# Kernel optimization log

Measured on AMD Instinct MI355X. Metric: run time of the kernel, lower is better.

The kernel has to match this reference:

```python
import jax, jax.numpy as jnp
import numpy as np

QUERY_DIM = 512
CTX_DIM = 1576
N_VIEWS = 36


def get_pano_affinity_np():
    pano_a = np.eye(36, dtype=np.float64)
    for v in range(0, 12):
        pano_a[v, v + 12] = 1
        if v == 0:
            pano_a[v, 11] = 1; pano_a[v, 11 + 12] = 1
        else:
            pano_a[v, v - 1] = 1; pano_a[v, v - 1 + 12] = 1
        if v == 11:
            pano_a[v, 0] = 1; pano_a[v, 0 + 12] = 1
        else:
            pano_a[v, v + 1] = 1; pano_a[v, v + 1 + 12] = 1
    for v in range(12, 24):
        pano_a[v, v + 12] = 1; pano_a[v, v - 12] = 1
        if v == 12:
            pano_a[v, 23] = 1; pano_a[v, 23 + 12] = 1; pano_a[v, 23 - 12] = 1
        else:
            pano_a[v, v - 1] = 1; pano_a[v, v - 1 + 12] = 1; pano_a[v, v - 1 - 12] = 1
        if v == 23:
            pano_a[v, 12] = 1; pano_a[v, 12 + 12] = 1; pano_a[v, 12 - 12] = 1
        else:
            pano_a[v, v + 1] = 1; pano_a[v, v + 1 + 12] = 1; pano_a[v, v + 1 - 12] = 1
    for v in range(24, 36):
        pano_a[v, v - 12] = 1
        if v == 24:
            pano_a[v, 35] = 1; pano_a[v, 35 - 12] = 1
        else:
            pano_a[v, v - 1] = 1; pano_a[v, v - 1 - 12] = 1
        if v == 35:
            pano_a[v, 24] = 1; pano_a[v, 24 - 12] = 1
        else:
            pano_a[v, v + 1] = 1; pano_a[v, v + 1 - 12] = 1
    # cv.GaussianBlur((3,3), sigma=0) uses fixed kernel [0.25,0.5,0.25];
    # BORDER_TRANSPARENT leaves border pixels unchanged.
    h = pano_a[:, :-2] * 0.25 + pano_a[:, 1:-1] * 0.5 + pano_a[:, 2:] * 0.25
    v2 = h[:-2] * 0.25 + h[1:-1] * 0.5 + h[2:] * 0.25
    out = pano_a.copy()
    out[1:-1, 1:-1] = v2
    out[np.eye(36, dtype=bool)] = 1.0
    out = out.astype(np.float32)
    out[out == 0] = 0.01
    return out


def setup_inputs() -> dict:
    key = jax.random.key(0)
    ks = jax.random.split(key, 8)
    B, L = 128, 8
    Q = jax.random.normal(ks[0], (B, L, QUERY_DIM), dtype=jnp.float32)
    V = jax.random.normal(ks[1], (B, L, N_VIEWS, CTX_DIM), dtype=jnp.float32)
    detect_feats = jax.random.normal(ks[2], (B, L, 900), dtype=jnp.float32)
    knowledge_vector = jax.random.normal(ks[3], (B, L, 112), dtype=jnp.float32)
    teacher_action_view_ids = jax.random.randint(ks[4], (B, L), 0, N_VIEWS, dtype=jnp.int64 if jax.config.jax_enable_x64 else jnp.int32)
    W_key = 0.02 * jax.random.normal(ks[5], (QUERY_DIM, 2476), dtype=jnp.float32)
    W_query = 0.02 * jax.random.normal(ks[6], (QUERY_DIM, QUERY_DIM), dtype=jnp.float32)
    W_out = 0.02 * jax.random.normal(ks[7], (QUERY_DIM, QUERY_DIM + CTX_DIM + 112), dtype=jnp.float32)
    return {"Q": Q, "V": V, "detect_feats": detect_feats,
            "knowledge_vector": knowledge_vector,
            "teacher_action_view_ids": teacher_action_view_ids,
            "W_key": W_key, "W_query": W_query, "W_out": W_out}


def reference(Q, V, detect_feats, knowledge_vector, teacher_action_view_ids,
              W_key, W_query, W_out):
    pano_a = jnp.asarray(get_pano_affinity_np())  # [36,36]
    B, L, qd = Q.shape
    ba = B * L
    Qf = Q.reshape(ba, qd) @ W_query.T                      # [ba, qd]
    Vf = V.reshape(ba, N_VIEWS, CTX_DIM)                    # [ba, 36, ctx]
    df = detect_feats.reshape(ba, 900)
    kv = knowledge_vector.reshape(ba, 112)
    tid = teacher_action_view_ids.reshape(ba)
    # K = Linear(cat(V, detect)) ; split the matmul to avoid materializing cat
    Wk_v, Wk_d = W_key[:, :CTX_DIM], W_key[:, CTX_DIM:]
    K = jnp.einsum('bnc,qc->bnq', Vf, Wk_v) + (df @ Wk_d.T)[:, None, :]  # [ba,36,qd]
    energy = jnp.einsum('bnq,bq->bn', K, Qf)                # [ba, 36]
    scale = qd ** (-0.5)
    attn = jax.nn.softmax(energy * scale, axis=1)           # [ba, 36]
    pano_tea = jax.lax.stop_gradient(pano_a[tid])           # [ba, 36]
    attn_gcn = attn * pano_tea
    weighted_context = jnp.einsum('bn,bnc->bc', attn_gcn, Vf)  # [ba, ctx]
    h = jnp.concatenate([weighted_context, Qf, kv], axis=1)
    h_tilde = jnp.tanh(h @ W_out.T)                         # [ba, qd]
    return (h_tilde, attn)
```

## Files before the change

kernel.cpp:

```cpp
#include <hip/hip_runtime.h>
#include <hip/hip_bf16.h>
#include <math.h>

typedef float f32x4 __attribute__((ext_vector_type(4)));
typedef short short8 __attribute__((ext_vector_type(8)));
typedef short short4v __attribute__((ext_vector_type(4)));

#define BA 1024
#define QD 512
#define CD 1576
#define NV 36
#define KVD 112
#define HLD 2200
#define WKLD 2476
#define CD4 394
#define LDP 72

__device__ __forceinline__ float pano_adj(int v, int w) {
    if (v == w) return 1.f;
    int rv = v / 12, rw = w / 12;
    int dr = rv - rw; if (dr < 0) dr = -dr;
    if (dr > 1) return 0.f;
    int dc = ((v % 12) - (w % 12) + 12) % 12;
    if (dc == 1 || dc == 11) return 1.f;
    if (dc == 0 && dr == 1) return 1.f;
    return 0.f;
}

__device__ __forceinline__ float pano_entry(int i, int j) {
    if (i == j) return 1.0f;
    float val;
    if (i >= 1 && i <= 34 && j >= 1 && j <= 34) {
        float wr[3] = {0.25f, 0.5f, 0.25f};
        val = 0.f;
        #pragma unroll
        for (int di = 0; di < 3; ++di)
            #pragma unroll
            for (int dj = 0; dj < 3; ++dj)
                val += wr[di] * wr[dj] * pano_adj(i - 1 + di, j - 1 + dj);
    } else {
        val = pano_adj(i, j);
    }
    return (val == 0.f) ? 0.01f : val;
}

__device__ __forceinline__ short f2bf(float f) {
    __hip_bfloat16 h = __float2bfloat16(f);
    union { __hip_bfloat16 b; short s; } u; u.b = h; return u.s;
}

template<bool ABF16, bool BBF16, bool CBF16, bool TANH>
__device__ void gemm_tile64(const void* __restrict__ Av, const void* __restrict__ Bv,
                            void* __restrict__ Cv, int m0, int n0, int N, int K,
                            int lda, int ldb, int ldc,
                            short* __restrict__ As, short* __restrict__ Bs) {
    const int t = threadIdx.x;
    const int lane = t & 63, w = t >> 6;
    const float* Af = (const float*)Av; const short* Ah = (const short*)Av;
    const float* Bf = (const float*)Bv; const short* Bh = (const short*)Bv;

    const int ar = t >> 3, akq = (t & 7) * 8;

    short8 abuf, bbuf;

    auto loadA = [&](int k0) {
        const size_t ro = (size_t)(m0 + ar) * lda;
        const int k = k0 + akq;
        short8 z;
        if (ABF16) {
            if (k + 8 <= K) z = *(const short8*)(Ah + ro + k);
            else {
                #pragma unroll
                for (int j = 0; j < 8; ++j) z[j] = (k + j < K) ? Ah[ro + k + j] : (short)0;
            }
        } else {
            if (k + 8 <= K) {
                f32x4 v0 = *(const f32x4*)(Af + ro + k);
                f32x4 v1 = *(const f32x4*)(Af + ro + k + 4);
                z[0]=f2bf(v0.x); z[1]=f2bf(v0.y); z[2]=f2bf(v0.z); z[3]=f2bf(v0.w);
                z[4]=f2bf(v1.x); z[5]=f2bf(v1.y); z[6]=f2bf(v1.z); z[7]=f2bf(v1.w);
            } else {
                #pragma unroll
                for (int j = 0; j < 8; ++j) z[j] = (k + j < K) ? f2bf(Af[ro + k + j]) : (short)0;
            }
        }
        abuf = z;
    };
    auto loadB = [&](int k0) {
        const int rn = n0 + ar;
        const size_t ro = (size_t)rn * ldb;
        const bool ok = rn < N;
        const int k = k0 + akq;
        short8 z;
        if (BBF16) {
            if (ok && k + 8 <= K) z = *(const short8*)(Bh + ro + k);
            else {
                #pragma unroll
                for (int j = 0; j < 8; ++j) z[j] = (ok && k + j < K) ? Bh[ro + k + j] : (short)0;
            }
        } else {
            if (ok && k + 8 <= K) {
                f32x4 v0 = *(const f32x4*)(Bf + ro + k);
                f32x4 v1 = *(const f32x4*)(Bf + ro + k + 4);
                z[0]=f2bf(v0.x); z[1]=f2bf(v0.y); z[2]=f2bf(v0.z); z[3]=f2bf(v0.w);
                z[4]=f2bf(v1.x); z[5]=f2bf(v1.y); z[6]=f2bf(v1.z); z[7]=f2bf(v1.w);
            } else {
                #pragma unroll
                for (int j = 0; j < 8; ++j) z[j] = (ok && k + j < K) ? f2bf(Bf[ro + k + j]) : (short)0;
            }
        }
        bbuf = z;
    };
    auto writeAB = [&](int buf) {
        *(short8*)&As[buf * (64 * LDP) + ar * LDP + akq] = abuf;
        *(short8*)&Bs[buf * (64 * LDP) + ar * LDP + akq] = bbuf;
    };

    const int wm = (w >> 2) * 32;
    const int wn = (w & 3) * 16;
    const int kb = (lane >> 4) * 8;
    int aidx[2], bidx;
    #pragma unroll
    for (int i = 0; i < 2; ++i)
        aidx[i] = (wm + i * 16 + (lane & 15)) * LDP + kb;
    bidx = (wn + (lane & 15)) * LDP + kb;

    f32x4 acc[2];
    #pragma unroll
    for (int i = 0; i < 2; ++i) acc[i] = (f32x4){0.f, 0.f, 0.f, 0.f};

    const int nk = (K + 63) / 64;
    loadA(0); loadB(0); writeAB(0);
    __syncthreads();

    int cur = 0;
    for (int kt = 0; kt < nk; ++kt) {
        const bool more = (kt + 1 < nk);
        if (more) { loadA((kt + 1) * 64); loadB((kt + 1) * 64); }

        #pragma unroll
        for (int ks = 0; ks < 2; ++ks) {
            short8 bfr = *(short8*)&Bs[cur * (64 * LDP) + bidx + ks * 32];
            #pragma unroll
            for (int i = 0; i < 2; ++i) {
                short8 afr = *(short8*)&As[cur * (64 * LDP) + aidx[i] + ks * 32];
                acc[i] = __builtin_amdgcn_mfma_f32_16x16x32_bf16(afr, bfr, acc[i], 0, 0, 0);
            }
        }
        if (more) writeAB(cur ^ 1);
        __syncthreads();
        cur ^= 1;
    }

    #pragma unroll
    for (int i = 0; i < 2; ++i) {
        int row = m0 + wm + i * 16 + (lane >> 4) * 4;
        int col = n0 + wn + (lane & 15);
        if (col < N) {
            #pragma unroll
            for (int r = 0; r < 4; ++r) {
                float v = acc[i][r];
                if (TANH) v = tanhf(v);
                if (CBF16) ((short*)Cv)[(size_t)(row + r) * ldc + col] = f2bf(v);
                else       ((float*)Cv)[(size_t)(row + r) * ldc + col] = v;
            }
        }
    }
}

__global__ __launch_bounds__(512) void gemm1_prep(
        const float* __restrict__ Q, const float* __restrict__ Wq,
        const float* __restrict__ Wk, const float* __restrict__ Wo,
        short* __restrict__ h, short* __restrict__ wk_t,
        short* __restrict__ wo_b) {
    __shared__ __align__(16) short As[2][64 * LDP];
    __shared__ __align__(16) short Bs[2][64 * LDP];
    __shared__ float tile[32][33];
    const int bx = blockIdx.x, t = threadIdx.x;

    if (bx < 128) {
        gemm_tile64<false, false, true, false>(
            (const void*)Q, (const void*)Wq, (void*)(h + CD),
            (bx >> 3) * 64, (bx & 7) * 64, QD, QD,
            QD, QD, HLD, &As[0][0], &Bs[0][0]);
    } else if (bx < 328) {
        const int pb = bx - 128;
        const int tx = t & 31, ty = t >> 5;
        for (int it = pb; it < 800; it += 200) {
            const int n0 = (it % 50) * 32, q0 = (it / 50) * 32;
            #pragma unroll
            for (int i = 0; i < 2; ++i)
                tile[ty + i * 16][tx] =
                    Wk[(size_t)(q0 + ty + i * 16) * WKLD + n0 + tx];
            __syncthreads();
            #pragma unroll
            for (int i = 0; i < 2; ++i) {
                int n = n0 + ty + i * 16;
                if (n < CD)
                    wk_t[(size_t)n * QD + q0 + tx] = f2bf(tile[tx][ty + i * 16]);
            }
            __syncthreads();
        }
    } else {
        const int NWO4 = (QD * HLD) / 4;
        for (int i = (bx - 328) * 512 + t; i < NWO4; i += 56 * 512) {
            f32x4 v4 = ((const f32x4*)Wo)[i];
            short4v o = { f2bf(v4.x), f2bf(v4.y), f2bf(v4.z), f2bf(v4.w) };
            ((short4v*)wo_b)[i] = o;
        }
    }
}

__global__ __launch_bounds__(256) void gemm2_nt(
        const short* __restrict__ Ah, const short* __restrict__ Bt,
        float* __restrict__ C, int M, int N, int K,
        int lda, int ldb, int ldc) {
    __shared__ __align__(16) short As[2][64 * LDP];
    __shared__ __align__(16) short Bs[2][64 * LDP];
    const int t = threadIdx.x;
    const int lane = t & 63, w = t >> 6;
    const int m0 = blockIdx.y * 64, n0 = blockIdx.x * 64;

    const int ar = t >> 2, akq = (t & 3) * 16;
    const int br = t >> 2, bkq = (t & 3) * 16;

    short8 abuf[2], bbuf[2];

    auto loadA = [&](int k0) {
        const size_t ro = (size_t)(m0 + ar) * lda;
        #pragma unroll
        for (int g = 0; g < 2; ++g) {
            int k = k0 + akq + g * 8;
            short8 z;
            if (k + 8 <= K) z = *(const short8*)(Ah + ro + k);
            else {
                #pragma unroll
                for (int j = 0; j < 8; ++j) z[j] = (k + j < K) ? Ah[ro + k + j] : (short)0;
            }
            abuf[g] = z;
        }
    };
    auto loadB = [&](int k0) {
        const int rn = n0 + br;
        const size_t ro = (size_t)rn * ldb;
        const bool ok = rn < N;
        #pragma unroll
        for (int g = 0; g < 2; ++g) {
            int k = k0 + bkq + g * 8;
            short8 z;
            if (ok && k + 8 <= K) z = *(const short8*)(Bt + ro + k);
            else {
                #pragma unroll
                for (int j = 0; j < 8; ++j) z[j] = (ok && k + j < K) ? Bt[ro + k + j] : (short)0;
            }
            bbuf[g] = z;
        }
    };
    auto writeAB = [&](int buf) {
        #pragma unroll
        for (int g = 0; g < 2; ++g) {
            *(short8*)&As[buf][ar * LDP + akq + g * 8] = abuf[g];
            *(short8*)&Bs[buf][br * LDP + bkq + g * 8] = bbuf[g];
        }
    };

    const int wm = (w >> 1) * 32, wn = (w & 1) * 32;
    const int kb = (lane >> 4) * 8;
    int aidx[2], bidx[2];
    #pragma unroll
    for (int i = 0; i < 2; ++i) {
        aidx[i] = (wm + i * 16 + (lane & 15)) * LDP + kb;
        bidx[i] = (wn + i * 16 + (lane & 15)) * LDP + kb;
    }

    f32x4 acc[2][2];
    #pragma unroll
    for (int i = 0; i < 2; ++i)
        #pragma unroll
        for (int j = 0; j < 2; ++j) acc[i][j] = (f32x4){0.f, 0.f, 0.f, 0.f};

    const int nk = (K + 63) / 64;
    loadA(0); loadB(0); writeAB(0);
    __syncthreads();

    int cur = 0;
    for (int kt = 0; kt < nk; ++kt) {
        const bool more = (kt + 1 < nk);
        if (more) { loadA((kt + 1) * 64); loadB((kt + 1) * 64); }

        #pragma unroll
        for (int ks = 0; ks < 2; ++ks) {
            short8 afr[2], bfr[2];
            #pragma unroll
            for (int i = 0; i < 2; ++i) afr[i] = *(short8*)&As[cur][aidx[i] + ks * 32];
            #pragma unroll
            for (int j = 0; j < 2; ++j) bfr[j] = *(short8*)&Bs[cur][bidx[j] + ks * 32];
            #pragma unroll
            for (int i = 0; i < 2; ++i)
                #pragma unroll
                for (int j = 0; j < 2; ++j)
                    acc[i][j] = __builtin_amdgcn_mfma_f32_16x16x32_bf16(afr[i], bfr[j], acc[i][j], 0, 0, 0);
        }
        if (more) writeAB(cur ^ 1);
        __syncthreads();
        cur ^= 1;
    }

    #pragma unroll
    for (int i = 0; i < 2; ++i) {
        #pragma unroll
        for (int j = 0; j < 2; ++j) {
            int row = m0 + wm + i * 16 + (lane >> 4) * 4;
            int col = n0 + wn + j * 16 + (lane & 15);
            if (col < N) {
                #pragma unroll
                for (int r = 0; r < 4; ++r)
                    C[(size_t)(row + r) * ldc + col] = acc[i][j][r];
            }
        }
    }
}

#define NR 5
#define NCH 7
__global__ __launch_bounds__(512, 2) void attn_wc_multib(
        const float* __restrict__ V, const float* __restrict__ P,
        const int* __restrict__ tid, const float* __restrict__ kv,
        short* __restrict__ h, float* __restrict__ attn_out) {
    const int t = threadIdx.x;
    const int w = t >> 6, lane = t & 63;
    __shared__ float en[NV];
    __shared__ float ag[NV];
    __shared__ __align__(16) f32x4 part[8 * 448];

    f32x4 p[NCH];
    f32x4 v[NR][NCH];

    auto issue_loads = [&](int b) {
        const f32x4* V4 = (const f32x4*)(V + (size_t)b * NV * CD);
        const f32x4* P4 = (const f32x4*)(P + (size_t)b * CD);
        #pragma unroll
        for (int j = 0; j < NCH; ++j) {
            int c = lane + 64 * j;
            p[j] = (c < CD4) ? P4[c] : (f32x4){0.f, 0.f, 0.f, 0.f};
        }
        #pragma unroll
        for (int r = 0; r < NR; ++r) {
            int n = w + 8 * r;
            #pragma unroll
            for (int j = 0; j < NCH; ++j) {
                int c = lane + 64 * j;
                v[r][j] = (n < NV && c < CD4) ? V4[(size_t)n * CD4 + c]
                                              : (f32x4){0.f, 0.f, 0.f, 0.f};
            }
        }
    };

    issue_loads(blockIdx.x * 4);

    for (int bi = 0; bi < 4; ++bi) {
        const int b = blockIdx.x * 4 + bi;

        #pragma unroll
        for (int r = 0; r < NR; ++r) {
            float s = 0.f;
            #pragma unroll
            for (int j = 0; j < NCH; ++j) {
                f32x4 vv = v[r][j], pp = p[j];
                s += vv.x * pp.x + vv.y * pp.y + vv.z * pp.z + vv.w * pp.w;
            }
            #pragma unroll
            for (int off = 32; off > 0; off >>= 1) s += __shfl_xor(s, off);
            int n = w + 8 * r;
            if (lane == 0 && n < NV) en[n] = s;
        }
        __syncthreads();

        if (t < 64) {
            const float SCALE = 0.044194173824159216f;
            float e = (t < NV) ? en[t] * SCALE : -1e30f;
            float m = e;
            #pragma unroll
            for (int off = 32; off > 0; off >>= 1) m = fmaxf(m, __shfl_xor(m, off));
            float pr = (t < NV) ? __expf(e - m) : 0.f;
            float s = pr;
            #pragma unroll
            for (int off = 32; off > 0; off >>= 1) s += __shfl_xor(s, off);
            float a = pr / s;
            if (t < NV) {
                attn_out[(size_t)b * NV + t] = a;
                ag[t] = a * pano_entry(tid[b], t);
            }
        }
        __syncthreads();

        f32x4 acc[NCH];
        #pragma unroll
        for (int j = 0; j < NCH; ++j) acc[j] = (f32x4){0.f, 0.f, 0.f, 0.f};
        #pragma unroll
        for (int r = 0; r < NR; ++r) {
            int n = w + 8 * r;
            float a = (n < NV) ? ag[n] : 0.f;
            #pragma unroll
            for (int j = 0; j < NCH; ++j) {
                acc[j].x += a * v[r][j].x; acc[j].y += a * v[r][j].y;
                acc[j].z += a * v[r][j].z; acc[j].w += a * v[r][j].w;
            }
        }
        #pragma unroll
        for (int j = 0; j < NCH; ++j)
            part[w * 448 + lane + 64 * j] = acc[j];

        if (bi < 3) issue_loads(b + 1);
        __syncthreads();

        short* hb = h + (size_t)b * HLD;
        if (t < CD4) {
            f32x4 s = part[t];
            #pragma unroll
            for (int w2 = 1; w2 < 8; ++w2) {
                f32x4 q = part[w2 * 448 + t];
                s.x += q.x; s.y += q.y; s.z += q.z; s.w += q.w;
            }
            short4v o = { f2bf(s.x), f2bf(s.y), f2bf(s.z), f2bf(s.w) };
            *(short4v*)(hb + t * 4) = o;
        }
        if (t < KVD)
            hb[CD + QD + t] = f2bf(kv[(size_t)b * KVD + t]);
    }
}

__global__ __launch_bounds__(256) void gemm4_tanh(
        const short* __restrict__ A, const short* __restrict__ B,
        float* __restrict__ C) {
    __shared__ __align__(16) short As[2][32 * LDP];
    __shared__ __align__(16) short Bs[2][32 * LDP];
    const int t = threadIdx.x;
    const int lane = t & 63, w = t >> 6;
    const int n0 = blockIdx.x * 32, m0 = blockIdx.y * 32;
    const int sr = t >> 3, skq = (t & 7) * 8;
    const int K = HLD;

    short8 abuf, bbuf;
    auto load = [&](int k0) {
        int k = k0 + skq;
        const short* pa = A + (size_t)(m0 + sr) * HLD + k;
        const short* pb = B + (size_t)(n0 + sr) * HLD + k;
        short8 za, zb;
        if (k + 8 <= K) { za = *(const short8*)pa; zb = *(const short8*)pb; }
        else {
            #pragma unroll
            for (int j = 0; j < 8; ++j) {
                za[j] = (k + j < K) ? pa[j] : (short)0;
                zb[j] = (k + j < K) ? pb[j] : (short)0;
            }
        }
        abuf = za; bbuf = zb;
    };
    auto write = [&](int buf) {
        *(short8*)&As[buf][sr * LDP + skq] = abuf;
        *(short8*)&Bs[buf][sr * LDP + skq] = bbuf;
    };

    const int wm = (w >> 1) * 16, wn = (w & 1) * 16;
    const int kb = (lane >> 4) * 8;
    const int aidx = (wm + (lane & 15)) * LDP + kb;
    const int bidx = (wn + (lane & 15)) * LDP + kb;

    f32x4 acc = {0.f, 0.f, 0.f, 0.f};
    const int nk = (K + 63) / 64;
    load(0); write(0);
    __syncthreads();

    int cur = 0;
    for (int kt = 0; kt < nk; ++kt) {
        const bool more = (kt + 1 < nk);
        if (more) load((kt + 1) * 64);

        #pragma unroll
        for (int ks = 0; ks < 2; ++ks) {
            short8 afr = *(short8*)&As[cur][aidx + ks * 32];
            short8 bfr = *(short8*)&Bs[cur][bidx + ks * 32];
            acc = __builtin_amdgcn_mfma_f32_16x16x32_bf16(afr, bfr, acc, 0, 0, 0);
        }
        if (more) write(cur ^ 1);
        __syncthreads();
        cur ^= 1;
    }

    const int row = m0 + wm + (lane >> 4) * 4;
    const int col = n0 + wn + (lane & 15);
    #pragma unroll
    for (int r = 0; r < 4; ++r)
        C[(size_t)(row + r) * QD + col] = tanhf(acc[r]);
}

extern "C" void kernel_launch(void* const* d_in, const int* in_sizes, int n_in,
                              void* d_out, int out_size, void* d_ws, size_t ws_size,
                              hipStream_t stream) {
    const float* Q   = (const float*)d_in[0];
    const float* V   = (const float*)d_in[1];
    const float* kv  = (const float*)d_in[3];
    const int*   tid = (const int*)  d_in[4];
    const float* Wk  = (const float*)d_in[5];
    const float* Wq  = (const float*)d_in[6];
    const float* Wo  = (const float*)d_in[7];

    short* h    = (short*)d_ws;
    float* P    = (float*)(h + (size_t)BA * HLD);
    short* wk_t = (short*)(P + (size_t)BA * CD);
    short* wo_b = wk_t + (size_t)CD * QD;

    float* out      = (float*)d_out;
    float* attn_out = out + (size_t)BA * QD;

    gemm1_prep<<<384, 512, 0, stream>>>(Q, Wq, Wk, Wo, h, wk_t, wo_b);

    gemm2_nt<<<dim3((CD + 63) / 64, BA / 64), 256, 0, stream>>>(
        h + CD, wk_t, P, BA, CD, QD, HLD, QD, CD);

    attn_wc_multib<<<BA / 4, 512, 0, stream>>>(V, P, tid, kv, h, attn_out);

    gemm4_tanh<<<dim3(QD / 32, BA / 32), 256, 0, stream>>>(h, wo_b, out);
}
```

Before: 89.63 us.

## Precompute Qf/kv part of output GEMM alongside key projection; store P as bf16

Splits the final output GEMM so the [Qf, kv] slice of W_out is multiplied in the same launch as the key-projection GEMM. gemm4 then only runs over the 1576-wide weighted-context slice and seeds its accumulator from the precomputed partial. The projected-query matrix P is now stored in bf16, which halves its write and read traffic in the attention kernel but loses some precision in the energies. The kv bf16 packing also moves into the prep kernel.

```diff
diff --git a/kernel.cpp b/kernel.cpp
--- a/kernel.cpp
+++ b/kernel.cpp
@@ -14,6 +14,7 @@
 #define HLD 2200
 #define WKLD 2476
 #define CD4 394
+#define QKLD 624
 #define LDP 72
 
 __device__ __forceinline__ float pano_adj(int v, int w) {
@@ -49,11 +50,23 @@
     union { __hip_bfloat16 b; short s; } u; u.b = h; return u.s;
 }
 
+__device__ __forceinline__ f32x4 bf4f(short4v s) {
+    f32x4 r;
+    #pragma unroll
+    for (int i = 0; i < 4; ++i) {
+        union { unsigned u; float f; } c;
+        c.u = ((unsigned)(unsigned short)s[i]) << 16;
+        r[i] = c.f;
+    }
+    return r;
+}
+
 template<bool ABF16, bool BBF16, bool CBF16, bool TANH>
-__device__ void gemm_tile64(const void* __restrict__ Av, const void* __restrict__ Bv,
-                            void* __restrict__ Cv, int m0, int n0, int N, int K,
-                            int lda, int ldb, int ldc,
-                            short* __restrict__ As, short* __restrict__ Bs) {
+__device__ __forceinline__ void gemm_tile64(
+        const void* __restrict__ Av, const void* __restrict__ Bv,
+        void* __restrict__ Cv, int m0, int n0, int N, int K,
+        int lda, int ldb, int ldc,
+        short* __restrict__ As, short* __restrict__ Bs) {
     const int t = threadIdx.x;
     const int lane = t & 63, w = t >> 6;
     const float* Af = (const float*)Av; const short* Ah = (const short*)Av;
@@ -171,18 +184,18 @@
 __global__ __launch_bounds__(512) void gemm1_prep(
         const float* __restrict__ Q, const float* __restrict__ Wq,
         const float* __restrict__ Wk, const float* __restrict__ Wo,
-        short* __restrict__ h, short* __restrict__ wk_t,
+        const float* __restrict__ kv,
+        short* __restrict__ qfkv, short* __restrict__ wk_t,
         short* __restrict__ wo_b) {
-    __shared__ __align__(16) short As[2][64 * LDP];
-    __shared__ __align__(16) short Bs[2][64 * LDP];
+    __shared__ __align__(16) short As[2 * 64 * LDP];
+    __shared__ __align__(16) short Bs[2 * 64 * LDP];
     __shared__ float tile[32][33];
     const int bx = blockIdx.x, t = threadIdx.x;
 
     if (bx < 128) {
         gemm_tile64<false, false, true, false>(
-            (const void*)Q, (const void*)Wq, (void*)(h + CD),
-            (bx >> 3) * 64, (bx & 7) * 64, QD, QD,
-            QD, QD, HLD, &As[0][0], &Bs[0][0]);
+            (const void*)Q, (const void*)Wq, (void*)qfkv,
+            (bx >> 3) * 64, (bx & 7) * 64, QD, QD, QD, QD, QKLD, As, Bs);
     } else if (bx < 328) {
         const int pb = bx - 128;
         const int tx = t & 31, ty = t >> 5;
@@ -208,21 +221,26 @@
             short4v o = { f2bf(v4.x), f2bf(v4.y), f2bf(v4.z), f2bf(v4.w) };
             ((short4v*)wo_b)[i] = o;
         }
-    }
-}
-
-__global__ __launch_bounds__(256) void gemm2_nt(
+        const int NKV4 = (BA * KVD) / 4;
+        for (int i = (bx - 328) * 512 + t; i < NKV4; i += 56 * 512) {
+            int b = i / 28, off = (i % 28) * 4;
+            f32x4 v4 = *(const f32x4*)(kv + (size_t)b * KVD + off);
+            short4v o = { f2bf(v4.x), f2bf(v4.y), f2bf(v4.z), f2bf(v4.w) };
+            *(short4v*)(qfkv + (size_t)b * QKLD + QD + off) = o;
+        }
+    }
+}
+
+template<bool CBF16>
+__device__ __forceinline__ void gemm_nt256(
         const short* __restrict__ Ah, const short* __restrict__ Bt,
-        float* __restrict__ C, int M, int N, int K,
-        int lda, int ldb, int ldc) {
-    __shared__ __align__(16) short As[2][64 * LDP];
-    __shared__ __align__(16) short Bs[2][64 * LDP];
+        void* __restrict__ Cv, int m0, int n0, int N, int K,
+        int lda, int ldb, int ldc,
+        short (*As)[64 * LDP], short (*Bs)[64 * LDP]) {
     const int t = threadIdx.x;
     const int lane = t & 63, w = t >> 6;
-    const int m0 = blockIdx.y * 64, n0 = blockIdx.x * 64;
 
     const int ar = t >> 2, akq = (t & 3) * 16;
-    const int br = t >> 2, bkq = (t & 3) * 16;
 
     short8 abuf[2], bbuf[2];
 
@@ -241,12 +259,12 @@
         }
     };
     auto loadB = [&](int k0) {
-        const int rn = n0 + br;
+        const int rn = n0 + ar;
         const size_t ro = (size_t)rn * ldb;
         const bool ok = rn < N;
         #pragma unroll
         for (int g = 0; g < 2; ++g) {
-            int k = k0 + bkq + g * 8;
+            int k = k0 + akq + g * 8;
             short8 z;
             if (ok && k + 8 <= K) z = *(const short8*)(Bt + ro + k);
             else {
@@ -260,7 +278,7 @@
         #pragma unroll
         for (int g = 0; g < 2; ++g) {
             *(short8*)&As[buf][ar * LDP + akq + g * 8] = abuf[g];
-            *(short8*)&Bs[buf][br * LDP + bkq + g * 8] = bbuf[g];
+            *(short8*)&Bs[buf][ar * LDP + akq + g * 8] = bbuf[g];
         }
     };
 
@@ -314,19 +332,40 @@
             int col = n0 + wn + j * 16 + (lane & 15);
             if (col < N) {
                 #pragma unroll
-                for (int r = 0; r < 4; ++r)
-                    C[(size_t)(row + r) * ldc + col] = acc[i][j][r];
-            }
-        }
+                for (int r = 0; r < 4; ++r) {
+                    if (CBF16) ((short*)Cv)[(size_t)(row + r) * ldc + col] = f2bf(acc[i][j][r]);
+                    else       ((float*)Cv)[(size_t)(row + r) * ldc + col] = acc[i][j][r];
+                }
+            }
+        }
+    }
+}
+
+__global__ __launch_bounds__(256) void gemm2pre(
+        const short* __restrict__ qfkv, const short* __restrict__ wk_t,
+        const short* __restrict__ wo_b, short* __restrict__ Pb,
+        float* __restrict__ pre) {
+    __shared__ __align__(16) short As[2][64 * LDP];
+    __shared__ __align__(16) short Bs[2][64 * LDP];
+    const int bx = blockIdx.x;
+    if (bx < 400) {
+        gemm_nt256<true>(qfkv, wk_t, (void*)Pb,
+                         (bx / 25) * 64, (bx % 25) * 64, CD, QD,
+                         QKLD, QD, CD, As, Bs);
+    } else {
+        const int j = bx - 400;
+        gemm_nt256<false>(qfkv, wo_b + CD, (void*)pre,
+                          (j >> 3) * 64, (j & 7) * 64, QD, QKLD,
+                          QKLD, HLD, QD, As, Bs);
     }
 }
 
 #define NR 5
 #define NCH 7
 __global__ __launch_bounds__(512, 2) void attn_wc_multib(
-        const float* __restrict__ V, const float* __restrict__ P,
-        const int* __restrict__ tid, const float* __restrict__ kv,
-        short* __restrict__ h, float* __restrict__ attn_out) {
+        const float* __restrict__ V, const short* __restrict__ Pb,
+        const int* __restrict__ tid, short* __restrict__ wc,
+        float* __restrict__ attn_out) {
     const int t = threadIdx.x;
     const int w = t >> 6, lane = t & 63;
     __shared__ float en[NV];
@@ -336,14 +375,8 @@
     f32x4 p[NCH];
     f32x4 v[NR][NCH];
 
-    auto issue_loads = [&](int b) {
+    auto load_v = [&](int b) {
         const f32x4* V4 = (const f32x4*)(V + (size_t)b * NV * CD);
-        const f32x4* P4 = (const f32x4*)(P + (size_t)b * CD);
-        #pragma unroll
-        for (int j = 0; j < NCH; ++j) {
-            int c = lane + 64 * j;
-            p[j] = (c < CD4) ? P4[c] : (f32x4){0.f, 0.f, 0.f, 0.f};
-        }
         #pragma unroll
         for (int r = 0; r < NR; ++r) {
             int n = w + 8 * r;
@@ -355,8 +388,17 @@
             }
         }
     };
-
-    issue_loads(blockIdx.x * 4);
+    auto load_p = [&](int b) {
+        const short4v* P4 = (const short4v*)(Pb + (size_t)b * CD);
+        #pragma unroll
+        for (int j = 0; j < NCH; ++j) {
+            int c = lane + 64 * j;
+            p[j] = (c < CD4) ? bf4f(P4[c]) : (f32x4){0.f, 0.f, 0.f, 0.f};
+        }
+    };
+
+    load_v(blockIdx.x * 4);
+    load_p(blockIdx.x * 4);
 
     for (int bi = 0; bi < 4; ++bi) {
         const int b = blockIdx.x * 4 + bi;
@@ -411,10 +453,10 @@
         for (int j = 0; j < NCH; ++j)
             part[w * 448 + lane + 64 * j] = acc[j];
 
-        if (bi < 3) issue_loads(b + 1);
+        if (bi < 3) { load_p(b + 1); load_v(b + 1); }
         __syncthreads();
 
-        short* hb = h + (size_t)b * HLD;
+        short* hb = wc + (size_t)b * CD;
         if (t < CD4) {
             f32x4 s = part[t];
             #pragma unroll
@@ -425,26 +467,24 @@
             short4v o = { f2bf(s.x), f2bf(s.y), f2bf(s.z), f2bf(s.w) };
             *(short4v*)(hb + t * 4) = o;
         }
-        if (t < KVD)
-            hb[CD + QD + t] = f2bf(kv[(size_t)b * KVD + t]);
     }
 }
 
 __global__ __launch_bounds__(256) void gemm4_tanh(
         const short* __restrict__ A, const short* __restrict__ B,
-        float* __restrict__ C) {
+        const float* __restrict__ pre, float* __restrict__ C) {
     __shared__ __align__(16) short As[2][32 * LDP];
     __shared__ __align__(16) short Bs[2][32 * LDP];
     const int t = threadIdx.x;
     const int lane = t & 63, w = t >> 6;
     const int n0 = blockIdx.x * 32, m0 = blockIdx.y * 32;
     const int sr = t >> 3, skq = (t & 7) * 8;
-    const int K = HLD;
+    const int K = CD;
 
     short8 abuf, bbuf;
     auto load = [&](int k0) {
         int k = k0 + skq;
-        const short* pa = A + (size_t)(m0 + sr) * HLD + k;
+        const short* pa = A + (size_t)(m0 + sr) * CD + k;
         const short* pb = B + (size_t)(n0 + sr) * HLD + k;
         short8 za, zb;
         if (k + 8 <= K) { za = *(const short8*)pa; zb = *(const short8*)pb; }
@@ -467,7 +507,13 @@
     const int aidx = (wm + (lane & 15)) * LDP + kb;
     const int bidx = (wn + (lane & 15)) * LDP + kb;
 
-    f32x4 acc = {0.f, 0.f, 0.f, 0.f};
+    const int row = m0 + wm + (lane >> 4) * 4;
+    const int col = n0 + wn + (lane & 15);
+    f32x4 acc;
+    #pragma unroll
+    for (int r = 0; r < 4; ++r)
+        acc[r] = pre[(size_t)(row + r) * QD + col];
+
     const int nk = (K + 63) / 64;
     load(0); write(0);
     __syncthreads();
@@ -488,8 +534,6 @@
         cur ^= 1;
     }
 
-    const int row = m0 + wm + (lane >> 4) * 4;
-    const int col = n0 + wn + (lane & 15);
     #pragma unroll
     for (int r = 0; r < 4; ++r)
         C[(size_t)(row + r) * QD + col] = tanhf(acc[r]);
@@ -506,20 +550,21 @@
     const float* Wq  = (const float*)d_in[6];
     const float* Wo  = (const float*)d_in[7];
 
-    short* h    = (short*)d_ws;
-    float* P    = (float*)(h + (size_t)BA * HLD);
-    short* wk_t = (short*)(P + (size_t)BA * CD);
+    short* qfkv = (short*)d_ws;
+    short* wc   = qfkv + (size_t)BA * QKLD;
+    short* Pb   = wc   + (size_t)BA * CD;
+    short* wk_t = Pb   + (size_t)BA * CD;
     short* wo_b = wk_t + (size_t)CD * QD;
+    float* pre  = (float*)(wo_b + (size_t)QD * HLD);
 
     float* out      = (float*)d_out;
     float* attn_out = out + (size_t)BA * QD;
 
-    gemm1_prep<<<384, 512, 0, stream>>>(Q, Wq, Wk, Wo, h, wk_t, wo_b);
-
-    gemm2_nt<<<dim3((CD + 63) / 64, BA / 64), 256, 0, stream>>>(
-        h + CD, wk_t, P, BA, CD, QD, HLD, QD, CD);
-
-    attn_wc_multib<<<BA / 4, 512, 0, stream>>>(V, P, tid, kv, h, attn_out);
-
-    gemm4_tanh<<<dim3(QD / 32, BA / 32), 256, 0, stream>>>(h, wo_b, out);
-}
+    gemm1_prep<<<384, 512, 0, stream>>>(Q, Wq, Wk, Wo, kv, qfkv, wk_t, wo_b);
+
+    gemm2pre<<<528, 256, 0, stream>>>(qfkv, wk_t, wo_b, Pb, pre);
+
+    attn_wc_multib<<<BA / 4, 512, 0, stream>>>(V, Pb, tid, wc, attn_out);
+
+    gemm4_tanh<<<dim3(QD / 32, BA / 32), 256, 0, stream>>>(wc, wo_b, pre, out);
+}
```

Result: faster. 82.48 us (median of 2 runs) (-8.0%).
